# Kernel optimization log

Measured on AMD Instinct MI355X. Metric: run time of the kernel, lower is better.

## Reference

```python
import jax, jax.numpy as jnp
import numpy as np

M, N, D, P, N_kv = 512, 4096, 128, 3584, 1024
H, H_kv = N // D, N_kv // D          # 32 query heads, 8 kv heads
G = H // H_kv                        # group size 4
L = P + M                            # cache length 4096


def setup_inputs() -> dict:
    key = jax.random.key(0)
    ks = jax.random.split(key, 6)
    w_scale = 0.008  # ~0.5/sqrt(N): keeps unscaled exp-softmax logits in fp32 range
    return {
        "X": jax.random.normal(ks[0], (M, N), jnp.float32),
        "W_q": jax.random.normal(ks[1], (N, N), jnp.float32) * w_scale,
        "W_k": jax.random.normal(ks[2], (N, N_kv), jnp.float32) * w_scale,
        "W_v": jax.random.normal(ks[3], (N, N_kv), jnp.float32) * w_scale,
        "cache_K": jax.random.normal(ks[4], (H, L, D), jnp.float32) * 0.02,
        "cache_V": jax.random.normal(ks[5], (H, L, D), jnp.float32) * 0.02,
    }


def reference(X, W_q, W_k, W_v, cache_K, cache_V):
    # fused QKV projection
    W_qkv = jnp.concatenate([W_q, W_k, W_v], axis=1)        # [N, N + 2*N_kv]
    qkv = X @ W_qkv                                          # [M, N + 2*N_kv]
    q = qkv[:, :N].reshape(M, H, D).transpose(1, 0, 2)       # [H, M, D]
    k = qkv[:, N:N + N_kv].reshape(M, H_kv, D).transpose(1, 0, 2)   # [H_kv, M, D]
    v = qkv[:, N + N_kv:].reshape(M, H_kv, D).transpose(1, 0, 2)    # [H_kv, M, D]
    # expand grouped KV heads (repeat_interleave) and append to cache at P
    k_exp = jnp.repeat(k, G, axis=0)                         # [H, M, D]
    v_exp = jnp.repeat(v, G, axis=0)
    Kc = cache_K.at[:, P:P + M, :].set(k_exp)                # [H, L, D]
    Vc = cache_V.at[:, P:P + M, :].set(v_exp)
    # naive (unscaled, non-max-subtracted) softmax attention over full cache
    scores = jnp.einsum('hmd,hld->hml', q, Kc)               # [H, M, L]
    e = jnp.exp(scores)
    weights = e / jnp.sum(e, axis=-1, keepdims=True)
    out = jnp.einsum('hml,hld->hmd', weights, Vc)            # [H, M, D]
    return out.transpose(1, 0, 2).reshape(M, H * D)          # [M, N]
```

## Files before the change

### kernel.cpp

```cpp
#include <hip/hip_runtime.h>

typedef __attribute__((ext_vector_type(8))) short short8;
typedef __attribute__((ext_vector_type(4))) float f32x4;

#define M_   512
#define N_   4096
#define D_   128
#define P_   3584
#define NKV  1024
#define L_   4096
#define H_   32

__device__ __forceinline__ ushort f2bf(float f) {
  union { float f; unsigned u; } v; v.f = f;
  unsigned r = (v.u + 0x7fffu + ((v.u >> 16) & 1u)) >> 16;
  return (ushort)r;
}
__device__ __forceinline__ float bf2f(ushort u) {
  union { unsigned u; float f; } v; v.u = ((unsigned)u) << 16;
  return v.f;
}

__device__ __forceinline__ void gload_lds16(const void* g, void* l) {
  __builtin_amdgcn_global_load_lds(
      (const __attribute__((address_space(1))) void*)g,
      (__attribute__((address_space(3))) void*)l, 16, 0, 0);
}

__global__ __launch_bounds__(256) void xconv(const float* __restrict__ X,
                                             ushort* __restrict__ Xs)
{
  int g = blockIdx.x * 256 + threadIdx.x;
  int row = g >> 9;
  int cir = g & 511;
  int grp = cir >> 3, ch = cir & 7;
  const float* src = &X[(size_t)row * 4096 + cir * 8];
  float4 f0 = *reinterpret_cast<const float4*>(src);
  float4 f1 = *reinterpret_cast<const float4*>(src + 4);
  short8 s;
  s[0] = f2bf(f0.x); s[1] = f2bf(f0.y); s[2] = f2bf(f0.z); s[3] = f2bf(f0.w);
  s[4] = f2bf(f1.x); s[5] = f2bf(f1.y); s[6] = f2bf(f1.z); s[7] = f2bf(f1.w);
  int dcol = grp * 64 + ((ch ^ (row & 7)) * 8);
  *reinterpret_cast<short8*>(&Xs[(size_t)row * 4096 + dcol]) = s;
}

__global__ __launch_bounds__(256) void wtrans(
    const float* __restrict__ Wq, const float* __restrict__ Wk,
    const float* __restrict__ Wv, ushort* __restrict__ Wt)
{
  int bx = blockIdx.x;
  int by = blockIdx.y;
  const float* W; int wcols, c0;
  if (by < 64)      { W = Wq; wcols = 4096; c0 = by * 64; }
  else if (by < 80) { W = Wk; wcols = 1024; c0 = (by - 64) * 64; }
  else              { W = Wv; wcols = 1024; c0 = (by - 80) * 64; }
  int orow0 = by * 64;
  int r0 = bx * 64;
  __shared__ float T[64][65];
  int tid = threadIdx.x;

  #pragma unroll
  for (int i = 0; i < 4; ++i) {
    int r = i * 16 + (tid >> 4);
    int c4 = tid & 15;
    float4 f = *reinterpret_cast<const float4*>(&W[(size_t)(r0 + r) * wcols + c0 + c4 * 4]);
    T[r][c4 * 4 + 0] = f.x; T[r][c4 * 4 + 1] = f.y;
    T[r][c4 * 4 + 2] = f.z; T[r][c4 * 4 + 3] = f.w;
  }
  __syncthreads();

  #pragma unroll
  for (int i = 0; i < 2; ++i) {
    int j = i * 256 + tid;
    int orr = j >> 3;
    int ch = j & 7;
    short8 s;
    #pragma unroll
    for (int e = 0; e < 8; ++e) s[e] = f2bf(T[ch * 8 + e][orr]);
    int orow = orow0 + orr;
    int dstch = ch ^ (orow & 7);
    *reinterpret_cast<short8*>(&Wt[(size_t)orow * 4096 + r0 + dstch * 8]) = s;
  }
}

#define GEMM_STAGE(buf, k0g) do {                                             \
    _Pragma("unroll")                                                         \
    for (int i_ = 0; i_ < 4; ++i_) {                                          \
      int blk_ = w * 4 + i_;                                                  \
      gload_lds16(Asrc + (size_t)(blk_ * 8 + (lane >> 3)) * 4096 + (k0g) + (lane & 7) * 8, \
                  &As[buf][blk_ * 512]);                                      \
    }                                                                         \
    _Pragma("unroll")                                                         \
    for (int i_ = 0; i_ < 4; ++i_) {                                          \
      int blk_ = w * 4 + i_;                                                  \
      gload_lds16(Bsrc + (size_t)(blk_ * 8 + (lane >> 3)) * 4096 + (k0g) + (lane & 7) * 8, \
                  &Bs[buf][blk_ * 512]);                                      \
    }                                                                         \
  } while (0)

__global__ __launch_bounds__(256, 2) void qkv_gemm3(
    const ushort* __restrict__ Xs, const ushort* __restrict__ Wt,
    float* __restrict__ pg)
{
  const int bx = blockIdx.x;
  const int by = blockIdx.y;
  const int bz = blockIdx.z;
  const int tid = threadIdx.x, lane = tid & 63, w = tid >> 6;
  const int wr = w >> 1, wc = w & 1;
  const int m0 = by * 128, n0 = bx * 128;
  const int kb0 = bz * 2048;

  __shared__ ushort As[2][128 * 64];
  __shared__ ushort Bs[2][128 * 64];

  f32x4 acc[4][4];
  #pragma unroll
  for (int m = 0; m < 4; ++m)
    #pragma unroll
    for (int n = 0; n < 4; ++n)
      acc[m][n] = (f32x4){0.f, 0.f, 0.f, 0.f};

  const ushort* Asrc = Xs + (size_t)m0 * 4096;
  const ushort* Bsrc = Wt + (size_t)n0 * 4096;

  GEMM_STAGE(0, kb0);
  __syncthreads();
  int cur = 0;

  for (int kt = 0; kt < 32; ++kt) {
    if (kt + 1 < 32) GEMM_STAGE(cur ^ 1, kb0 + (kt + 1) * 64);
    #pragma unroll
    for (int kk = 0; kk < 2; ++kk) {
      short8 a[4], b[4];
      #pragma unroll
      for (int m = 0; m < 4; ++m) {
        int row = wr * 64 + m * 16 + (lane & 15);
        int ch = (kk * 4 + (lane >> 4)) ^ (row & 7);
        a[m] = *reinterpret_cast<const short8*>(&As[cur][row * 64 + ch * 8]);
      }
      #pragma unroll
      for (int n = 0; n < 4; ++n) {
        int row = wc * 64 + n * 16 + (lane & 15);
        int ch = (kk * 4 + (lane >> 4)) ^ (row & 7);
        b[n] = *reinterpret_cast<const short8*>(&Bs[cur][row * 64 + ch * 8]);
      }
      #pragma unroll
      for (int m = 0; m < 4; ++m)
        #pragma unroll
        for (int n = 0; n < 4; ++n)
          acc[m][n] = __builtin_amdgcn_mfma_f32_16x16x32_bf16(a[m], b[n], acc[m][n], 0, 0, 0);
    }
    __syncthreads();
    cur ^= 1;
  }

  float* dst = pg + (size_t)bz * 512 * 6144;
  #pragma unroll
  for (int m = 0; m < 4; ++m)
    #pragma unroll
    for (int n = 0; n < 4; ++n)
      #pragma unroll
      for (int j = 0; j < 4; ++j) {
        int row = m0 + wr * 64 + m * 16 + (lane >> 4) * 4 + j;
        int col = n0 + wc * 64 + n * 16 + (lane & 15);
        dst[(size_t)row * 6144 + col] = acc[m][n][j];
      }
}

__global__ __launch_bounds__(256) void combine_qk(
    const float* __restrict__ pg, ushort* __restrict__ qb,
    ushort* __restrict__ Kb)
{
  int id = blockIdx.x * 256 + threadIdx.x;
  int m = id / 640;
  int c8 = (id - m * 640) * 8;
  const float* p0 = pg + (size_t)m * 6144 + c8;
  const float* p1 = p0 + (size_t)512 * 6144;
  short8 s;
  #pragma unroll
  for (int e = 0; e < 8; ++e) s[e] = f2bf(p0[e] + p1[e]);
  if (c8 < 4096) {
    *reinterpret_cast<short8*>(&qb[(size_t)m * 4096 + c8]) = s;
  } else {
    int o = c8 - 4096;
    int hk = o >> 7, d0 = o & 127;
    int l = P_ + m;
    int ch = (d0 >> 3) ^ (l & 7);
    #pragma unroll
    for (int g = 0; g < 4; ++g)
      *reinterpret_cast<short8*>(&Kb[((size_t)(hk * 4 + g) * L_ + l) * 128 + ch * 8]) = s;
  }
}

__global__ __launch_bounds__(256) void combine_v(
    const float* __restrict__ pg, ushort* __restrict__ Vtb)
{
  int bz = blockIdx.x;
  int mt = bz & 7, hk = (bz >> 3) & 7, dh = bz >> 6;
  int m0 = mt * 64, d0 = dh * 64;
  int colbase = 5120 + hk * 128 + d0;
  __shared__ float T[64][65];
  int tid = threadIdx.x;
  int r = tid >> 2, q4 = tid & 3;

  #pragma unroll
  for (int i = 0; i < 4; ++i) {
    int c = (q4 * 4 + i) * 4;
    const float* p0 = pg + (size_t)(m0 + r) * 6144 + colbase + c;
    const float* p1 = p0 + (size_t)512 * 6144;
    float4 a = *reinterpret_cast<const float4*>(p0);
    float4 b = *reinterpret_cast<const float4*>(p1);
    T[r][c + 0] = a.x + b.x; T[r][c + 1] = a.y + b.y;
    T[r][c + 2] = a.z + b.z; T[r][c + 3] = a.w + b.w;
  }
  __syncthreads();

  #pragma unroll
  for (int p = 0; p < 2; ++p) {
    int idx = p * 256 + tid;
    int dloc = idx >> 3, cc = idx & 7;
    int half = cc >> 2, c4 = (cc & 3) * 4;
    short8 s;
    #pragma unroll
    for (int e = 0; e < 8; ++e) {
      int lrow = half * 32 + c4 + (e < 4 ? e : 16 + (e - 4));
      s[e] = f2bf(T[lrow][dloc]);
    }
    int d = d0 + dloc;
    int pc = (cc & 4) | ((cc ^ (d >> 1)) & 3);
    int l0 = P_ + m0;
    #pragma unroll
    for (int g = 0; g < 4; ++g) {
      int h = hk * 4 + g;
      *reinterpret_cast<short8*>(&Vtb[((size_t)h * 128 + d) * (size_t)L_ + l0 + pc * 8]) = s;
    }
  }
}

__global__ __launch_bounds__(256) void kconv(
    const float* __restrict__ cacheK, ushort* __restrict__ Kb)
{
  int h = blockIdx.x, lt = blockIdx.y;
  int tid = threadIdx.x;
  int r = tid >> 4, c = tid & 15;
  int l = lt * 16 + r;
  const float* src = &cacheK[((size_t)h * L_ + l) * 128 + c * 8];
  float4 f0 = *reinterpret_cast<const float4*>(src);
  float4 f1 = *reinterpret_cast<const float4*>(src + 4);
  short8 s;
  s[0] = f2bf(f0.x); s[1] = f2bf(f0.y); s[2] = f2bf(f0.z); s[3] = f2bf(f0.w);
  s[4] = f2bf(f1.x); s[5] = f2bf(f1.y); s[6] = f2bf(f1.z); s[7] = f2bf(f1.w);
  int pc = c ^ (l & 7);
  *reinterpret_cast<short8*>(&Kb[((size_t)h * L_ + l) * 128 + pc * 8]) = s;
}

__global__ __launch_bounds__(256) void vconv(
    const float* __restrict__ cacheV, ushort* __restrict__ Vtb)
{
  int h = blockIdx.x, lt = blockIdx.y, dh = blockIdx.z;
  int l0 = lt * 64, d0 = dh * 64;
  __shared__ float T[64][65];
  int tid = threadIdx.x;
  int r4 = tid >> 4, c = tid & 15;

  #pragma unroll
  for (int p = 0; p < 4; ++p) {
    int r = p * 16 + r4;
    float4 f = *reinterpret_cast<const float4*>(
        &cacheV[((size_t)h * L_ + l0 + r) * 128 + d0 + c * 4]);
    T[r][c * 4 + 0] = f.x; T[r][c * 4 + 1] = f.y;
    T[r][c * 4 + 2] = f.z; T[r][c * 4 + 3] = f.w;
  }
  __syncthreads();

  int dr = tid >> 2, part = tid & 3;
  int d = d0 + dr;
  #pragma unroll
  for (int q = 0; q < 2; ++q) {
    int cc = part * 2 + q;
    int half = cc >> 2, c4 = (cc & 3) * 4;
    short8 s;
    #pragma unroll
    for (int e = 0; e < 8; ++e) {
      int lrow = half * 32 + c4 + (e < 4 ? e : 16 + (e - 4));
      s[e] = f2bf(T[lrow][dr]);
    }
    int pc = (cc & 4) | ((cc ^ (d >> 1)) & 3);
    *reinterpret_cast<short8*>(&Vtb[((size_t)h * 128 + d) * (size_t)L_ + l0 + pc * 8]) = s;
  }
}

#define ATTN_STAGE(buf, l0g) do {                                             \
    gload_lds16(&Kb[kbase + (size_t)((l0g) + w * 4 + (lane >> 4)) * 128 + (lane & 15) * 8], \
                &Ks[buf][(w * 4) * 128]);                                     \
    gload_lds16(&Vtb[vbase + (size_t)(w * 16 + (lane >> 2)) * (size_t)L_ + (l0g) + (lane & 3) * 8], \
                &Vt[buf][(w * 16) * 32]);                                     \
  } while (0)

#define ATTN_TILE(bufc) do {                                                  \
    const ushort* Ksb = &Ks[bufc][0];                                         \
    const ushort* Vsb = &Vt[bufc][0];                                         \
    f32x4 sc0 = (f32x4){0.f, 0.f, 0.f, 0.f};                                  \
    f32x4 sc1 = (f32x4){0.f, 0.f, 0.f, 0.f};                                  \
    __builtin_amdgcn_s_setprio(1);                                            \
    _Pragma("unroll")                                                         \
    for (int kk = 0; kk < 4; ++kk) {                                          \
      int ch = (kk * 4 + hi) ^ (lo16 & 7);                                    \
      short8 a0 = *reinterpret_cast<const short8*>(&Ksb[lo16 * 128 + ch * 8]); \
      short8 a1 = *reinterpret_cast<const short8*>(&Ksb[(16 + lo16) * 128 + ch * 8]); \
      sc0 = __builtin_amdgcn_mfma_f32_16x16x32_bf16(a0, qreg[kk], sc0, 0, 0, 0); \
      sc1 = __builtin_amdgcn_mfma_f32_16x16x32_bf16(a1, qreg[kk], sc1, 0, 0, 0); \
    }                                                                         \
    __builtin_amdgcn_s_setprio(0);                                            \
    short8 pa;                                                                \
    {                                                                         \
      float e0 = __expf(sc0[0]); float e1 = __expf(sc0[1]);                   \
      float e2 = __expf(sc0[2]); float e3 = __expf(sc0[3]);                   \
      float f0 = __expf(sc1[0]); float f1 = __expf(sc1[1]);                   \
      float f2 = __expf(sc1[2]); float f3 = __expf(sc1[3]);                   \
      rs += ((e0 + e1) + (e2 + e3)) + ((f0 + f1) + (f2 + f3));                \
      pa[0] = f2bf(e0); pa[1] = f2bf(e1); pa[2] = f2bf(e2); pa[3] = f2bf(e3); \
      pa[4] = f2bf(f0); pa[5] = f2bf(f1); pa[6] = f2bf(f2); pa[7] = f2bf(f3); \
    }                                                                         \
    __builtin_amdgcn_s_setprio(1);                                            \
    _Pragma("unroll")                                                         \
    for (int n = 0; n < 8; ++n) {                                             \
      int d = n * 16 + lo16;                                                  \
      int chv = hi ^ ((d >> 1) & 3);                                          \
      short8 bn = *reinterpret_cast<const short8*>(&Vsb[d * 32 + chv * 8]);   \
      o[n] = __builtin_amdgcn_mfma_f32_16x16x32_bf16(pa, bn, o[n], 0, 0, 0);  \
    }                                                                         \
    __builtin_amdgcn_s_setprio(0);                                            \
  } while (0)

__global__ __launch_bounds__(512, 4) void gqa_attn8(
    const ushort* __restrict__ qb, const ushort* __restrict__ Kb,
    const ushort* __restrict__ Vtb,
    ushort* __restrict__ pob, float* __restrict__ prs)
{
  const int b = blockIdx.x;
  const int s = b & 3;
  const int j = b >> 2;
  const int qt = j & 3;
  const int h = j >> 2;
  const int tid = threadIdx.x, lane = tid & 63, w = tid >> 6;
  const int lo16 = lane & 15, hi = lane >> 4;

  __shared__ ushort Ks[4][32 * 128];
  __shared__ ushort Vt[4][128 * 32];

  short8 qreg[4];
  {
    int qrow = qt * 128 + w * 16 + lo16;
    #pragma unroll
    for (int kk = 0; kk < 4; ++kk)
      qreg[kk] = *reinterpret_cast<const short8*>(
          &qb[(size_t)qrow * 4096 + h * 128 + (kk * 4 + hi) * 8]);
  }

  f32x4 o[8];
  #pragma unroll
  for (int n = 0; n < 8; ++n)
    o[n] = (f32x4){0.f, 0.f, 0.f, 0.f};
  float rs = 0.f;

  const size_t kbase = ((size_t)h * L_ + s * 1024) * 128;
  const size_t vbase = (size_t)h * 128 * (size_t)L_ + s * 1024;

  ATTN_STAGE(0, 0);
  ATTN_STAGE(1, 32);
  asm volatile("s_waitcnt vmcnt(2)" ::: "memory");
  __builtin_amdgcn_s_barrier();

  for (int t = 0; t < 30; ++t) {
    ATTN_STAGE((t + 2) & 3, (t + 2) * 32);
    ATTN_TILE(t & 3);
    asm volatile("s_waitcnt vmcnt(2)" ::: "memory");
    __builtin_amdgcn_s_barrier();
  }
  ATTN_TILE(2);
  asm volatile("s_waitcnt vmcnt(0)" ::: "memory");
  __builtin_amdgcn_s_barrier();
  ATTN_TILE(3);

  float rsum = rs;
  rsum += __shfl_xor(rsum, 16, 64);
  rsum += __shfl_xor(rsum, 32, 64);

  const size_t pbase = (size_t)(s * 32 + h) * 512;
  #pragma unroll
  for (int n = 0; n < 8; ++n)
    #pragma unroll
    for (int j2 = 0; j2 < 4; ++j2) {
      int row = qt * 128 + w * 16 + hi * 4 + j2;
      pob[(pbase + row) * 128 + n * 16 + lo16] = f2bf(o[n][j2]);
    }
  if (hi == 0) {
    int row = qt * 128 + w * 16 + lo16;
    prs[pbase + row] = rsum;
  }
}

__global__ __launch_bounds__(256) void reduce_out(
    const ushort* __restrict__ pob, const float* __restrict__ prs,
    float* __restrict__ out)
{
  int id = blockIdx.x * 256 + threadIdx.x;
  int m = id >> 10, dq = id & 1023;
  int h = dq >> 5, d4 = dq & 31;
  float4 acc = {0.f, 0.f, 0.f, 0.f};
  float rsum = 0.f;
  #pragma unroll
  for (int s = 0; s < 4; ++s) {
    size_t base = (size_t)(s * 32 + h) * 512 + m;
    ushort4 v = *reinterpret_cast<const ushort4*>(&pob[base * 128 + d4 * 4]);
    acc.x += bf2f(v.x); acc.y += bf2f(v.y); acc.z += bf2f(v.z); acc.w += bf2f(v.w);
    rsum += prs[base];
  }
  float inv = 1.f / rsum;
  float4 r; r.x = acc.x * inv; r.y = acc.y * inv; r.z = acc.z * inv; r.w = acc.w * inv;
  *reinterpret_cast<float4*>(&out[(size_t)m * 4096 + dq * 4]) = r;
}

extern "C" void kernel_launch(void* const* d_in, const int* in_sizes, int n_in,
                              void* d_out, int out_size, void* d_ws, size_t ws_size,
                              hipStream_t stream) {
  const float* X  = (const float*)d_in[0];
  const float* Wq = (const float*)d_in[1];
  const float* Wk = (const float*)d_in[2];
  const float* Wv = (const float*)d_in[3];
  const float* cK = (const float*)d_in[4];
  const float* cV = (const float*)d_in[5];
  float* out = (float*)d_out;

  ushort* qb  = (ushort*)d_ws;
  ushort* Xs  = qb  + (size_t)M_ * N_;
  ushort* Kb  = Xs  + (size_t)M_ * N_;
  ushort* Vtb = Kb  + (size_t)H_ * L_ * D_;
  float*  prs = (float*)(Vtb + (size_t)H_ * L_ * D_);
  ushort* Wt  = (ushort*)(prs + 8 * 32 * 512);
  float*  pg  = (float*)(Wt + (size_t)6144 * 4096);
  ushort* pob = Wt;

  xconv<<<1024, 256, 0, stream>>>(X, Xs);
  wtrans<<<dim3(64, 96), 256, 0, stream>>>(Wq, Wk, Wv, Wt);
  qkv_gemm3<<<dim3(48, 4, 2), 256, 0, stream>>>(Xs, Wt, pg);
  combine_qk<<<1280, 256, 0, stream>>>(pg, qb, Kb);
  combine_v<<<128, 256, 0, stream>>>(pg, Vtb);
  kconv<<<dim3(32, 224), 256, 0, stream>>>(cK, Kb);
  vconv<<<dim3(32, 56, 2), 256, 0, stream>>>(cV, Vtb);
  gqa_attn8<<<512, 512, 0, stream>>>(qb, Kb, Vtb, pob, prs);
  reduce_out<<<2048, 256, 0, stream>>>(pob, prs, out);
}
```

Measured before the change: 170.5 us.

## Process two query fragments per wave and split KV length eight ways

```diff
diff --git a/kernel.cpp b/kernel.cpp
--- a/kernel.cpp
+++ b/kernel.cpp
@@ -300,27 +300,37 @@
 #define ATTN_TILE(bufc) do {                                                  \
     const ushort* Ksb = &Ks[bufc][0];                                         \
     const ushort* Vsb = &Vt[bufc][0];                                         \
-    f32x4 sc0 = (f32x4){0.f, 0.f, 0.f, 0.f};                                  \
-    f32x4 sc1 = (f32x4){0.f, 0.f, 0.f, 0.f};                                  \
+    f32x4 sc[2][2];                                                           \
+    _Pragma("unroll")                                                         \
+    for (int f = 0; f < 2; ++f)                                               \
+      _Pragma("unroll")                                                       \
+      for (int mb = 0; mb < 2; ++mb)                                          \
+        sc[f][mb] = (f32x4){0.f, 0.f, 0.f, 0.f};                              \
     __builtin_amdgcn_s_setprio(1);                                            \
     _Pragma("unroll")                                                         \
     for (int kk = 0; kk < 4; ++kk) {                                          \
       int ch = (kk * 4 + hi) ^ (lo16 & 7);                                    \
       short8 a0 = *reinterpret_cast<const short8*>(&Ksb[lo16 * 128 + ch * 8]); \
       short8 a1 = *reinterpret_cast<const short8*>(&Ksb[(16 + lo16) * 128 + ch * 8]); \
-      sc0 = __builtin_amdgcn_mfma_f32_16x16x32_bf16(a0, qreg[kk], sc0, 0, 0, 0); \
-      sc1 = __builtin_amdgcn_mfma_f32_16x16x32_bf16(a1, qreg[kk], sc1, 0, 0, 0); \
+      _Pragma("unroll")                                                       \
+      for (int f = 0; f < 2; ++f) {                                           \
+        sc[f][0] = __builtin_amdgcn_mfma_f32_16x16x32_bf16(a0, qreg[f][kk], sc[f][0], 0, 0, 0); \
+        sc[f][1] = __builtin_amdgcn_mfma_f32_16x16x32_bf16(a1, qreg[f][kk], sc[f][1], 0, 0, 0); \
+      }                                                                       \
     }                                                                         \
     __builtin_amdgcn_s_setprio(0);                                            \
-    short8 pa;                                                                \
-    {                                                                         \
-      float e0 = __expf(sc0[0]); float e1 = __expf(sc0[1]);                   \
-      float e2 = __expf(sc0[2]); float e3 = __expf(sc0[3]);                   \
-      float f0 = __expf(sc1[0]); float f1 = __expf(sc1[1]);                   \
-      float f2 = __expf(sc1[2]); float f3 = __expf(sc1[3]);                   \
-      rs += ((e0 + e1) + (e2 + e3)) + ((f0 + f1) + (f2 + f3));                \
-      pa[0] = f2bf(e0); pa[1] = f2bf(e1); pa[2] = f2bf(e2); pa[3] = f2bf(e3); \
-      pa[4] = f2bf(f0); pa[5] = f2bf(f1); pa[6] = f2bf(f2); pa[7] = f2bf(f3); \
+    short8 pa[2];                                                             \
+    _Pragma("unroll")                                                         \
+    for (int f = 0; f < 2; ++f) {                                             \
+      float e0 = __expf(sc[f][0][0]); float e1 = __expf(sc[f][0][1]);         \
+      float e2 = __expf(sc[f][0][2]); float e3 = __expf(sc[f][0][3]);         \
+      float g0 = __expf(sc[f][1][0]); float g1 = __expf(sc[f][1][1]);         \
+      float g2 = __expf(sc[f][1][2]); float g3 = __expf(sc[f][1][3]);         \
+      rs[f] += ((e0 + e1) + (e2 + e3)) + ((g0 + g1) + (g2 + g3));             \
+      pa[f][0] = f2bf(e0); pa[f][1] = f2bf(e1);                               \
+      pa[f][2] = f2bf(e2); pa[f][3] = f2bf(e3);                               \
+      pa[f][4] = f2bf(g0); pa[f][5] = f2bf(g1);                               \
+      pa[f][6] = f2bf(g2); pa[f][7] = f2bf(g3);                               \
     }                                                                         \
     __builtin_amdgcn_s_setprio(1);                                            \
     _Pragma("unroll")                                                         \
@@ -328,51 +338,55 @@
       int d = n * 16 + lo16;                                                  \
       int chv = hi ^ ((d >> 1) & 3);                                          \
       short8 bn = *reinterpret_cast<const short8*>(&Vsb[d * 32 + chv * 8]);   \
-      o[n] = __builtin_amdgcn_mfma_f32_16x16x32_bf16(pa, bn, o[n], 0, 0, 0);  \
+      o[0][n] = __builtin_amdgcn_mfma_f32_16x16x32_bf16(pa[0], bn, o[0][n], 0, 0, 0); \
+      o[1][n] = __builtin_amdgcn_mfma_f32_16x16x32_bf16(pa[1], bn, o[1][n], 0, 0, 0); \
     }                                                                         \
     __builtin_amdgcn_s_setprio(0);                                            \
   } while (0)
 
-__global__ __launch_bounds__(512, 4) void gqa_attn8(
+__global__ __launch_bounds__(512, 4) void gqa_attn10(
     const ushort* __restrict__ qb, const ushort* __restrict__ Kb,
     const ushort* __restrict__ Vtb,
     ushort* __restrict__ pob, float* __restrict__ prs)
 {
   const int b = blockIdx.x;
-  const int s = b & 3;
-  const int j = b >> 2;
-  const int qt = j & 3;
-  const int h = j >> 2;
+  const int s = b & 7;
+  const int j = b >> 3;
+  const int qt = j & 1;
+  const int h = j >> 1;
   const int tid = threadIdx.x, lane = tid & 63, w = tid >> 6;
   const int lo16 = lane & 15, hi = lane >> 4;
 
   __shared__ ushort Ks[4][32 * 128];
   __shared__ ushort Vt[4][128 * 32];
 
-  short8 qreg[4];
-  {
-    int qrow = qt * 128 + w * 16 + lo16;
+  short8 qreg[2][4];
+  #pragma unroll
+  for (int f = 0; f < 2; ++f) {
+    int qrow = qt * 256 + w * 32 + f * 16 + lo16;
     #pragma unroll
     for (int kk = 0; kk < 4; ++kk)
-      qreg[kk] = *reinterpret_cast<const short8*>(
+      qreg[f][kk] = *reinterpret_cast<const short8*>(
           &qb[(size_t)qrow * 4096 + h * 128 + (kk * 4 + hi) * 8]);
   }
 
-  f32x4 o[8];
-  #pragma unroll
-  for (int n = 0; n < 8; ++n)
-    o[n] = (f32x4){0.f, 0.f, 0.f, 0.f};
-  float rs = 0.f;
-
-  const size_t kbase = ((size_t)h * L_ + s * 1024) * 128;
-  const size_t vbase = (size_t)h * 128 * (size_t)L_ + s * 1024;
+  f32x4 o[2][8];
+  #pragma unroll
+  for (int f = 0; f < 2; ++f)
+    #pragma unroll
+    for (int n = 0; n < 8; ++n)
+      o[f][n] = (f32x4){0.f, 0.f, 0.f, 0.f};
+  float rs[2] = {0.f, 0.f};
+
+  const size_t kbase = ((size_t)h * L_ + s * 512) * 128;
+  const size_t vbase = (size_t)h * 128 * (size_t)L_ + s * 512;
 
   ATTN_STAGE(0, 0);
   ATTN_STAGE(1, 32);
   asm volatile("s_waitcnt vmcnt(2)" ::: "memory");
   __builtin_amdgcn_s_barrier();
 
-  for (int t = 0; t < 30; ++t) {
+  for (int t = 0; t < 14; ++t) {
     ATTN_STAGE((t + 2) & 3, (t + 2) * 32);
     ATTN_TILE(t & 3);
     asm volatile("s_waitcnt vmcnt(2)" ::: "memory");
@@ -383,21 +397,31 @@
   __builtin_amdgcn_s_barrier();
   ATTN_TILE(3);
 
-  float rsum = rs;
-  rsum += __shfl_xor(rsum, 16, 64);
-  rsum += __shfl_xor(rsum, 32, 64);
+  float rsum[2];
+  #pragma unroll
+  for (int f = 0; f < 2; ++f) {
+    float v = rs[f];
+    v += __shfl_xor(v, 16, 64);
+    v += __shfl_xor(v, 32, 64);
+    rsum[f] = v;
+  }
 
   const size_t pbase = (size_t)(s * 32 + h) * 512;
   #pragma unroll
-  for (int n = 0; n < 8; ++n)
-    #pragma unroll
-    for (int j2 = 0; j2 < 4; ++j2) {
-      int row = qt * 128 + w * 16 + hi * 4 + j2;
-      pob[(pbase + row) * 128 + n * 16 + lo16] = f2bf(o[n][j2]);
+  for (int f = 0; f < 2; ++f)
+    #pragma unroll
+    for (int n = 0; n < 8; ++n)
+      #pragma unroll
+      for (int j2 = 0; j2 < 4; ++j2) {
+        int row = qt * 256 + w * 32 + f * 16 + hi * 4 + j2;
+        pob[(pbase + row) * 128 + n * 16 + lo16] = f2bf(o[f][n][j2]);
+      }
+  if (hi == 0) {
+    #pragma unroll
+    for (int f = 0; f < 2; ++f) {
+      int row = qt * 256 + w * 32 + f * 16 + lo16;
+      prs[pbase + row] = rsum[f];
     }
-  if (hi == 0) {
-    int row = qt * 128 + w * 16 + lo16;
-    prs[pbase + row] = rsum;
   }
 }
 
@@ -411,7 +435,7 @@
   float4 acc = {0.f, 0.f, 0.f, 0.f};
   float rsum = 0.f;
   #pragma unroll
-  for (int s = 0; s < 4; ++s) {
+  for (int s = 0; s < 8; ++s) {
     size_t base = (size_t)(s * 32 + h) * 512 + m;
     ushort4 v = *reinterpret_cast<const ushort4*>(&pob[base * 128 + d4 * 4]);
     acc.x += bf2f(v.x); acc.y += bf2f(v.y); acc.z += bf2f(v.z); acc.w += bf2f(v.w);
@@ -449,6 +473,6 @@
   combine_v<<<128, 256, 0, stream>>>(pg, Vtb);
   kconv<<<dim3(32, 224), 256, 0, stream>>>(cK, Kb);
   vconv<<<dim3(32, 56, 2), 256, 0, stream>>>(cV, Vtb);
-  gqa_attn8<<<512, 512, 0, stream>>>(qb, Kb, Vtb, pob, prs);
+  gqa_attn10<<<512, 512, 0, stream>>>(qb, Kb, Vtb, pob, prs);
   reduce_out<<<2048, 256, 0, stream>>>(pob, prs, out);
 }
```

Result: slower. 187.9 us (+10.2%).

## Fuse weight transpose and bf16 conversion into the QKV GEMM

Applied to the files above, without the earlier changes.

```diff
diff --git a/kernel.cpp b/kernel.cpp
--- a/kernel.cpp
+++ b/kernel.cpp
@@ -44,62 +44,9 @@
   *reinterpret_cast<short8*>(&Xs[(size_t)row * 4096 + dcol]) = s;
 }
 
-__global__ __launch_bounds__(256) void wtrans(
-    const float* __restrict__ Wq, const float* __restrict__ Wk,
-    const float* __restrict__ Wv, ushort* __restrict__ Wt)
-{
-  int bx = blockIdx.x;
-  int by = blockIdx.y;
-  const float* W; int wcols, c0;
-  if (by < 64)      { W = Wq; wcols = 4096; c0 = by * 64; }
-  else if (by < 80) { W = Wk; wcols = 1024; c0 = (by - 64) * 64; }
-  else              { W = Wv; wcols = 1024; c0 = (by - 80) * 64; }
-  int orow0 = by * 64;
-  int r0 = bx * 64;
-  __shared__ float T[64][65];
-  int tid = threadIdx.x;
-
-  #pragma unroll
-  for (int i = 0; i < 4; ++i) {
-    int r = i * 16 + (tid >> 4);
-    int c4 = tid & 15;
-    float4 f = *reinterpret_cast<const float4*>(&W[(size_t)(r0 + r) * wcols + c0 + c4 * 4]);
-    T[r][c4 * 4 + 0] = f.x; T[r][c4 * 4 + 1] = f.y;
-    T[r][c4 * 4 + 2] = f.z; T[r][c4 * 4 + 3] = f.w;
-  }
-  __syncthreads();
-
-  #pragma unroll
-  for (int i = 0; i < 2; ++i) {
-    int j = i * 256 + tid;
-    int orr = j >> 3;
-    int ch = j & 7;
-    short8 s;
-    #pragma unroll
-    for (int e = 0; e < 8; ++e) s[e] = f2bf(T[ch * 8 + e][orr]);
-    int orow = orow0 + orr;
-    int dstch = ch ^ (orow & 7);
-    *reinterpret_cast<short8*>(&Wt[(size_t)orow * 4096 + r0 + dstch * 8]) = s;
-  }
-}
-
-#define GEMM_STAGE(buf, k0g) do {                                             \
-    _Pragma("unroll")                                                         \
-    for (int i_ = 0; i_ < 4; ++i_) {                                          \
-      int blk_ = w * 4 + i_;                                                  \
-      gload_lds16(Asrc + (size_t)(blk_ * 8 + (lane >> 3)) * 4096 + (k0g) + (lane & 7) * 8, \
-                  &As[buf][blk_ * 512]);                                      \
-    }                                                                         \
-    _Pragma("unroll")                                                         \
-    for (int i_ = 0; i_ < 4; ++i_) {                                          \
-      int blk_ = w * 4 + i_;                                                  \
-      gload_lds16(Bsrc + (size_t)(blk_ * 8 + (lane >> 3)) * 4096 + (k0g) + (lane & 7) * 8, \
-                  &Bs[buf][blk_ * 512]);                                      \
-    }                                                                         \
-  } while (0)
-
-__global__ __launch_bounds__(256, 2) void qkv_gemm3(
-    const ushort* __restrict__ Xs, const ushort* __restrict__ Wt,
+__global__ __launch_bounds__(256, 2) void qkv_gemm4(
+    const ushort* __restrict__ Xs, const float* __restrict__ Wq,
+    const float* __restrict__ Wk, const float* __restrict__ Wv,
     float* __restrict__ pg)
 {
   const int bx = blockIdx.x;
@@ -110,8 +57,14 @@
   const int m0 = by * 128, n0 = bx * 128;
   const int kb0 = bz * 2048;
 
-  __shared__ ushort As[2][128 * 64];
-  __shared__ ushort Bs[2][128 * 64];
+  const float* Wsrc; int wcols, c0;
+  if (n0 < 4096)      { Wsrc = Wq; wcols = 4096; c0 = n0; }
+  else if (n0 < 5120) { Wsrc = Wk; wcols = 1024; c0 = n0 - 4096; }
+  else                { Wsrc = Wv; wcols = 1024; c0 = n0 - 5120; }
+
+  __shared__ ushort As[128 * 64];
+  __shared__ ushort Bs[128 * 64];
+  __shared__ float  Tf[64 * 128];
 
   f32x4 acc[4][4];
   #pragma unroll
@@ -121,14 +74,57 @@
       acc[m][n] = (f32x4){0.f, 0.f, 0.f, 0.f};
 
   const ushort* Asrc = Xs + (size_t)m0 * 4096;
-  const ushort* Bsrc = Wt + (size_t)n0 * 4096;
-
-  GEMM_STAGE(0, kb0);
+
+  const int wr8 = tid >> 5;
+  const int wc4 = (tid & 31) * 4;
+  float4 wreg[8];
+
+#define WISSUE(kt_) do {                                                      \
+    _Pragma("unroll")                                                         \
+    for (int i_ = 0; i_ < 8; ++i_)                                            \
+      wreg[i_] = *reinterpret_cast<const float4*>(                            \
+          &Wsrc[(size_t)(kb0 + (kt_) * 64 + wr8 + 8 * i_) * wcols + c0 + wc4]); \
+  } while (0)
+
+#define WTF() do {                                                            \
+    _Pragma("unroll")                                                         \
+    for (int i_ = 0; i_ < 8; ++i_)                                            \
+      *reinterpret_cast<float4*>(&Tf[(wr8 + 8 * i_) * 128 + wc4]) = wreg[i_]; \
+  } while (0)
+
+#define BBUILD() do {                                                         \
+    _Pragma("unroll")                                                         \
+    for (int i_ = 0; i_ < 4; ++i_) {                                          \
+      int id_ = tid + 256 * i_;                                               \
+      int n_ = id_ & 127, cch_ = id_ >> 7;                                    \
+      short8 s_;                                                              \
+      _Pragma("unroll")                                                       \
+      for (int e_ = 0; e_ < 8; ++e_)                                          \
+        s_[e_] = f2bf(Tf[(cch_ * 8 + e_) * 128 + n_]);                        \
+      *reinterpret_cast<short8*>(&Bs[n_ * 64 + ((cch_ ^ (n_ & 7)) * 8)]) = s_; \
+    }                                                                         \
+  } while (0)
+
+#define ASTAGE(k0g) do {                                                      \
+    _Pragma("unroll")                                                         \
+    for (int i_ = 0; i_ < 4; ++i_) {                                          \
+      int blk_ = w * 4 + i_;                                                  \
+      gload_lds16(Asrc + (size_t)(blk_ * 8 + (lane >> 3)) * 4096 + (k0g) + (lane & 7) * 8, \
+                  &As[blk_ * 512]);                                           \
+    }                                                                         \
+  } while (0)
+
+  WISSUE(0);
+  WTF();
+  WISSUE(1);
   __syncthreads();
-  int cur = 0;
 
   for (int kt = 0; kt < 32; ++kt) {
-    if (kt + 1 < 32) GEMM_STAGE(cur ^ 1, kb0 + (kt + 1) * 64);
+    BBUILD();
+    ASTAGE(kb0 + kt * 64);
+    __syncthreads();
+    if (kt + 1 < 32) WTF();
+    if (kt + 2 < 32) WISSUE(kt + 2);
     #pragma unroll
     for (int kk = 0; kk < 2; ++kk) {
       short8 a[4], b[4];
@@ -136,13 +132,13 @@
       for (int m = 0; m < 4; ++m) {
         int row = wr * 64 + m * 16 + (lane & 15);
         int ch = (kk * 4 + (lane >> 4)) ^ (row & 7);
-        a[m] = *reinterpret_cast<const short8*>(&As[cur][row * 64 + ch * 8]);
+        a[m] = *reinterpret_cast<const short8*>(&As[row * 64 + ch * 8]);
       }
       #pragma unroll
       for (int n = 0; n < 4; ++n) {
         int row = wc * 64 + n * 16 + (lane & 15);
         int ch = (kk * 4 + (lane >> 4)) ^ (row & 7);
-        b[n] = *reinterpret_cast<const short8*>(&Bs[cur][row * 64 + ch * 8]);
+        b[n] = *reinterpret_cast<const short8*>(&Bs[row * 64 + ch * 8]);
       }
       #pragma unroll
       for (int m = 0; m < 4; ++m)
@@ -151,7 +147,6 @@
           acc[m][n] = __builtin_amdgcn_mfma_f32_16x16x32_bf16(a[m], b[n], acc[m][n], 0, 0, 0);
     }
     __syncthreads();
-    cur ^= 1;
   }
 
   float* dst = pg + (size_t)bz * 512 * 6144;
@@ -197,7 +192,9 @@
 {
   int bz = blockIdx.x;
   int mt = bz & 7, hk = (bz >> 3) & 7, dh = bz >> 6;
-  int m0 = mt * 64, d0 = dh * 64;
+  int m0 = bz & 7 ? mt * 64 : mt * 64;
+  m0 = mt * 64;
+  int d0 = dh * 64;
   int colbase = 5120 + hk * 128 + d0;
   __shared__ float T[64][65];
   int tid = threadIdx.x;
@@ -333,7 +330,7 @@
     __builtin_amdgcn_s_setprio(0);                                            \
   } while (0)
 
-__global__ __launch_bounds__(512, 4) void gqa_attn8(
+__global__ __launch_bounds__(512, 4) void gqa_attn11(
     const ushort* __restrict__ qb, const ushort* __restrict__ Kb,
     const ushort* __restrict__ Vtb,
     ushort* __restrict__ pob, float* __restrict__ prs)
@@ -438,17 +435,15 @@
   ushort* Kb  = Xs  + (size_t)M_ * N_;
   ushort* Vtb = Kb  + (size_t)H_ * L_ * D_;
   float*  prs = (float*)(Vtb + (size_t)H_ * L_ * D_);
-  ushort* Wt  = (ushort*)(prs + 8 * 32 * 512);
-  float*  pg  = (float*)(Wt + (size_t)6144 * 4096);
-  ushort* pob = Wt;
+  ushort* pob = (ushort*)(prs + 8 * 32 * 512);
+  float*  pg  = (float*)(pob + (size_t)6144 * 4096);
 
   xconv<<<1024, 256, 0, stream>>>(X, Xs);
-  wtrans<<<dim3(64, 96), 256, 0, stream>>>(Wq, Wk, Wv, Wt);
-  qkv_gemm3<<<dim3(48, 4, 2), 256, 0, stream>>>(Xs, Wt, pg);
+  qkv_gemm4<<<dim3(48, 4, 2), 256, 0, stream>>>(Xs, Wq, Wk, Wv, pg);
   combine_qk<<<1280, 256, 0, stream>>>(pg, qb, Kb);
   combine_v<<<128, 256, 0, stream>>>(pg, Vtb);
   kconv<<<dim3(32, 224), 256, 0, stream>>>(cK, Kb);
   vconv<<<dim3(32, 56, 2), 256, 0, stream>>>(cV, Vtb);
-  gqa_attn8<<<512, 512, 0, stream>>>(qb, Kb, Vtb, pob, prs);
+  gqa_attn11<<<512, 512, 0, stream>>>(qb, Kb, Vtb, pob, prs);
   reduce_out<<<2048, 256, 0, stream>>>(pob, prs, out);
 }
```

After: 263.4 us. 1.55x slower.

## Fuse fp32 KV-cache conversion into attention, dropping kconv/vconv kernels

Applied to the files above, without the earlier changes.

```diff
diff --git a/kernel.cpp b/kernel.cpp
--- a/kernel.cpp
+++ b/kernel.cpp
@@ -169,7 +169,7 @@
 
 __global__ __launch_bounds__(256) void combine_qk(
     const float* __restrict__ pg, ushort* __restrict__ qb,
-    ushort* __restrict__ Kb)
+    ushort* __restrict__ Kbn)
 {
   int id = blockIdx.x * 256 + threadIdx.x;
   int m = id / 640;
@@ -184,20 +184,19 @@
   } else {
     int o = c8 - 4096;
     int hk = o >> 7, d0 = o & 127;
-    int l = P_ + m;
-    int ch = (d0 >> 3) ^ (l & 7);
     #pragma unroll
     for (int g = 0; g < 4; ++g)
-      *reinterpret_cast<short8*>(&Kb[((size_t)(hk * 4 + g) * L_ + l) * 128 + ch * 8]) = s;
+      *reinterpret_cast<short8*>(&Kbn[((size_t)(hk * 4 + g) * 512 + m) * 128 + d0]) = s;
   }
 }
 
 __global__ __launch_bounds__(256) void combine_v(
-    const float* __restrict__ pg, ushort* __restrict__ Vtb)
+    const float* __restrict__ pg, ushort* __restrict__ Vtn)
 {
   int bz = blockIdx.x;
   int mt = bz & 7, hk = (bz >> 3) & 7, dh = bz >> 6;
-  int m0 = mt * 64, d0 = dh * 64;
+  int m0 = mt * 64;
+  int d0 = dh * 64;
   int colbase = 5120 + hk * 128 + d0;
   __shared__ float T[64][65];
   int tid = threadIdx.x;
@@ -227,75 +226,13 @@
       s[e] = f2bf(T[lrow][dloc]);
     }
     int d = d0 + dloc;
-    int pc = (cc & 4) | ((cc ^ (d >> 1)) & 3);
-    int l0 = P_ + m0;
     #pragma unroll
     for (int g = 0; g < 4; ++g) {
       int h = hk * 4 + g;
-      *reinterpret_cast<short8*>(&Vtb[((size_t)h * 128 + d) * (size_t)L_ + l0 + pc * 8]) = s;
+      *reinterpret_cast<short8*>(&Vtn[((size_t)h * 128 + d) * 512 + m0 + cc * 8]) = s;
     }
   }
 }
-
-__global__ __launch_bounds__(256) void kconv(
-    const float* __restrict__ cacheK, ushort* __restrict__ Kb)
-{
-  int h = blockIdx.x, lt = blockIdx.y;
-  int tid = threadIdx.x;
-  int r = tid >> 4, c = tid & 15;
-  int l = lt * 16 + r;
-  const float* src = &cacheK[((size_t)h * L_ + l) * 128 + c * 8];
-  float4 f0 = *reinterpret_cast<const float4*>(src);
-  float4 f1 = *reinterpret_cast<const float4*>(src + 4);
-  short8 s;
-  s[0] = f2bf(f0.x); s[1] = f2bf(f0.y); s[2] = f2bf(f0.z); s[3] = f2bf(f0.w);
-  s[4] = f2bf(f1.x); s[5] = f2bf(f1.y); s[6] = f2bf(f1.z); s[7] = f2bf(f1.w);
-  int pc = c ^ (l & 7);
-  *reinterpret_cast<short8*>(&Kb[((size_t)h * L_ + l) * 128 + pc * 8]) = s;
-}
-
-__global__ __launch_bounds__(256) void vconv(
-    const float* __restrict__ cacheV, ushort* __restrict__ Vtb)
-{
-  int h = blockIdx.x, lt = blockIdx.y, dh = blockIdx.z;
-  int l0 = lt * 64, d0 = dh * 64;
-  __shared__ float T[64][65];
-  int tid = threadIdx.x;
-  int r4 = tid >> 4, c = tid & 15;
-
-  #pragma unroll
-  for (int p = 0; p < 4; ++p) {
-    int r = p * 16 + r4;
-    float4 f = *reinterpret_cast<const float4*>(
-        &cacheV[((size_t)h * L_ + l0 + r) * 128 + d0 + c * 4]);
-    T[r][c * 4 + 0] = f.x; T[r][c * 4 + 1] = f.y;
-    T[r][c * 4 + 2] = f.z; T[r][c * 4 + 3] = f.w;
-  }
-  __syncthreads();
-
-  int dr = tid >> 2, part = tid & 3;
-  int d = d0 + dr;
-  #pragma unroll
-  for (int q = 0; q < 2; ++q) {
-    int cc = part * 2 + q;
-    int half = cc >> 2, c4 = (cc & 3) * 4;
-    short8 s;
-    #pragma unroll
-    for (int e = 0; e < 8; ++e) {
-      int lrow = half * 32 + c4 + (e < 4 ? e : 16 + (e - 4));
-      s[e] = f2bf(T[lrow][dr]);
-    }
-    int pc = (cc & 4) | ((cc ^ (d >> 1)) & 3);
-    *reinterpret_cast<short8*>(&Vtb[((size_t)h * 128 + d) * (size_t)L_ + l0 + pc * 8]) = s;
-  }
-}
-
-#define ATTN_STAGE(buf, l0g) do {                                             \
-    gload_lds16(&Kb[kbase + (size_t)((l0g) + w * 4 + (lane >> 4)) * 128 + (lane & 15) * 8], \
-                &Ks[buf][(w * 4) * 128]);                                     \
-    gload_lds16(&Vtb[vbase + (size_t)(w * 16 + (lane >> 2)) * (size_t)L_ + (l0g) + (lane & 3) * 8], \
-                &Vt[buf][(w * 16) * 32]);                                     \
-  } while (0)
 
 #define ATTN_TILE(bufc) do {                                                  \
     const ushort* Ksb = &Ks[bufc][0];                                         \
@@ -333,9 +270,43 @@
     __builtin_amdgcn_s_setprio(0);                                            \
   } while (0)
 
-__global__ __launch_bounds__(512, 4) void gqa_attn8(
-    const ushort* __restrict__ qb, const ushort* __restrict__ Kb,
-    const ushort* __restrict__ Vtb,
+#define AISSUE(t_) do {                                                       \
+    if (s3 && (t_) >= 16) {                                                   \
+      krn = *reinterpret_cast<const short8*>(                                 \
+          &KsrcN[(size_t)((t_) * 32 - 512 + klr) * 128 + kc * 8]);            \
+      vrn = *reinterpret_cast<const short8*>(                                 \
+          &VsrcN[(size_t)vd * 512 + ((t_) * 32 - 512) + vc3 * 8]);            \
+    } else {                                                                  \
+      const float* kp_ = &Ksrc[(size_t)((t_) * 32 + klr) * 128 + kc * 8];     \
+      kr0 = *reinterpret_cast<const float4*>(kp_);                            \
+      kr1 = *reinterpret_cast<const float4*>(kp_ + 4);                        \
+      _Pragma("unroll")                                                       \
+      for (int e_ = 0; e_ < 8; ++e_) {                                        \
+        int lr_ = (t_) * 32 + vc3 * 4 + (e_ < 4 ? e_ : 16 + (e_ - 4));        \
+        vr[e_] = Vsrc[(size_t)lr_ * 128 + vd];                                \
+      }                                                                       \
+    }                                                                         \
+  } while (0)
+
+#define AWRITE(t_) do {                                                       \
+    short8 ks_, vs_;                                                          \
+    if (s3 && (t_) >= 16) { ks_ = krn; vs_ = vrn; }                           \
+    else {                                                                    \
+      ks_[0] = f2bf(kr0.x); ks_[1] = f2bf(kr0.y);                             \
+      ks_[2] = f2bf(kr0.z); ks_[3] = f2bf(kr0.w);                             \
+      ks_[4] = f2bf(kr1.x); ks_[5] = f2bf(kr1.y);                             \
+      ks_[6] = f2bf(kr1.z); ks_[7] = f2bf(kr1.w);                             \
+      _Pragma("unroll")                                                       \
+      for (int e_ = 0; e_ < 8; ++e_) vs_[e_] = f2bf(vr[e_]);                  \
+    }                                                                         \
+    *reinterpret_cast<short8*>(&Ks[(t_) & 3][klr * 128 + ((kc ^ (klr & 7)) * 8)]) = ks_; \
+    *reinterpret_cast<short8*>(&Vt[(t_) & 3][vd * 32 + (((vc3 ^ (vd >> 1)) & 3) * 8)]) = vs_; \
+  } while (0)
+
+__global__ __launch_bounds__(512, 4) void gqa_attn12(
+    const ushort* __restrict__ qb, const float* __restrict__ cacheK,
+    const float* __restrict__ cacheV, const ushort* __restrict__ Kbn,
+    const ushort* __restrict__ Vtn,
     ushort* __restrict__ pob, float* __restrict__ prs)
 {
   const int b = blockIdx.x;
@@ -364,24 +335,31 @@
     o[n] = (f32x4){0.f, 0.f, 0.f, 0.f};
   float rs = 0.f;
 
-  const size_t kbase = ((size_t)h * L_ + s * 1024) * 128;
-  const size_t vbase = (size_t)h * 128 * (size_t)L_ + s * 1024;
-
-  ATTN_STAGE(0, 0);
-  ATTN_STAGE(1, 32);
-  asm volatile("s_waitcnt vmcnt(2)" ::: "memory");
+  const int klr = tid >> 4, kc = tid & 15;
+  const int vd = tid >> 2, vc3 = tid & 3;
+  const float* Ksrc = cacheK + ((size_t)h * L_ + s * 1024) * 128;
+  const float* Vsrc = cacheV + ((size_t)h * L_ + s * 1024) * 128;
+  const ushort* KsrcN = Kbn + (size_t)h * 512 * 128;
+  const ushort* VsrcN = Vtn + (size_t)h * 128 * 512;
+  const bool s3 = (s == 3);
+
+  float4 kr0, kr1;
+  float vr[8];
+  short8 krn, vrn;
+
+  AISSUE(0);
+  AWRITE(0);
+  AISSUE(1);
+  asm volatile("s_waitcnt lgkmcnt(0)" ::: "memory");
   __builtin_amdgcn_s_barrier();
 
-  for (int t = 0; t < 30; ++t) {
-    ATTN_STAGE((t + 2) & 3, (t + 2) * 32);
+  for (int t = 0; t < 32; ++t) {
+    if (t + 1 < 32) AWRITE(t + 1);
+    if (t + 2 < 32) AISSUE(t + 2);
     ATTN_TILE(t & 3);
-    asm volatile("s_waitcnt vmcnt(2)" ::: "memory");
+    asm volatile("s_waitcnt lgkmcnt(0)" ::: "memory");
     __builtin_amdgcn_s_barrier();
   }
-  ATTN_TILE(2);
-  asm volatile("s_waitcnt vmcnt(0)" ::: "memory");
-  __builtin_amdgcn_s_barrier();
-  ATTN_TILE(3);
 
   float rsum = rs;
   rsum += __shfl_xor(rsum, 16, 64);
@@ -435,20 +413,18 @@
 
   ushort* qb  = (ushort*)d_ws;
   ushort* Xs  = qb  + (size_t)M_ * N_;
-  ushort* Kb  = Xs  + (size_t)M_ * N_;
-  ushort* Vtb = Kb  + (size_t)H_ * L_ * D_;
-  float*  prs = (float*)(Vtb + (size_t)H_ * L_ * D_);
-  ushort* Wt  = (ushort*)(prs + 8 * 32 * 512);
+  ushort* Kbn = Xs  + (size_t)M_ * N_;
+  ushort* Vtn = Kbn + (size_t)H_ * 512 * D_;
+  float*  prs = (float*)(Vtn + (size_t)H_ * 512 * D_);
+  ushort* pob = (ushort*)(prs + 8 * 32 * 512);
+  ushort* Wt  = pob + (size_t)4 * H_ * 512 * D_;
   float*  pg  = (float*)(Wt + (size_t)6144 * 4096);
-  ushort* pob = Wt;
 
   xconv<<<1024, 256, 0, stream>>>(X, Xs);
   wtrans<<<dim3(64, 96), 256, 0, stream>>>(Wq, Wk, Wv, Wt);
   qkv_gemm3<<<dim3(48, 4, 2), 256, 0, stream>>>(Xs, Wt, pg);
-  combine_qk<<<1280, 256, 0, stream>>>(pg, qb, Kb);
-  combine_v<<<128, 256, 0, stream>>>(pg, Vtb);
-  kconv<<<dim3(32, 224), 256, 0, stream>>>(cK, Kb);
-  vconv<<<dim3(32, 56, 2), 256, 0, stream>>>(cV, Vtb);
-  gqa_attn8<<<512, 512, 0, stream>>>(qb, Kb, Vtb, pob, prs);
+  combine_qk<<<1280, 256, 0, stream>>>(pg, qb, Kbn);
+  combine_v<<<128, 256, 0, stream>>>(pg, Vtn);
+  gqa_attn12<<<512, 512, 0, stream>>>(qb, cK, cV, Kbn, Vtn, pob, prs);
   reduce_out<<<2048, 256, 0, stream>>>(pob, prs, out);
 }
```

Result: no change. 169.7 us (-0.4%).
